# Kernel tuning notes

Hardware: AMD Instinct MI355X
Metric: run time of the kernel (lower is better)

The kernel has to match this reference:

```python
import jax, jax.numpy as jnp
import numpy as np

S = 3072      # total packed tokens
D = 1536      # hidden_size
H = 12        # num_heads
HD = D // H   # head_dim = 128
NSEQ = 4      # number of packed sequences (images)


def rotate_half(x):
    x1 = x[..., : x.shape[-1] // 2]
    x2 = x[..., x.shape[-1] // 2 :]
    return jnp.concatenate((-x2, x1), axis=-1)


def setup_inputs() -> dict:
    key = jax.random.key(0)
    k1, k2, k3 = jax.random.split(key, 3)
    hidden_states = jax.random.normal(k1, (S, D), jnp.float32)
    # 4 equal-length packed sequences
    cu_seqlens = (jnp.arange(NSEQ + 1, dtype=jnp.int32) * (S // NSEQ))
    # RoPE cos/sin per token, period within each packed sequence
    pos = (jnp.arange(S) % (S // NSEQ)).astype(jnp.float32)
    inv_freq = 1.0 / (10000.0 ** (jnp.arange(0, HD // 2, dtype=jnp.float32) / (HD // 2)))
    freqs = pos[:, None] * inv_freq[None, :]          # [S, HD//2]
    emb = jnp.concatenate([freqs, freqs], axis=-1)    # [S, HD]
    cos, sin = jnp.cos(emb), jnp.sin(emb)
    qkv_w = jax.random.normal(k2, (3 * D, D), jnp.float32) * (D ** -0.5)
    qkv_b = jnp.zeros((3 * D,), jnp.float32)
    proj_w = jax.random.normal(k3, (D, D), jnp.float32) * (D ** -0.5)
    return {
        "hidden_states": hidden_states,
        "cos": cos,
        "sin": sin,
        "qkv_w": qkv_w,
        "qkv_b": qkv_b,
        "proj_w": proj_w,
        "cu_seqlens": cu_seqlens,
    }


def reference(hidden_states, cos, sin, qkv_w, qkv_b, proj_w, cu_seqlens):
    s_len, dim = hidden_states.shape
    # fused QKV projection -> [S, 3, H, HD]
    qkv = (hidden_states @ qkv_w.T + qkv_b).reshape(s_len, 3, H, HD)
    q, k, v = qkv[:, 0], qkv[:, 1], qkv[:, 2]         # each [S, H, HD]
    # inline RoPE (fp32, broadcast over heads)
    c = cos[:, None, :].astype(jnp.float32)
    s = sin[:, None, :].astype(jnp.float32)
    qf, kf = q.astype(jnp.float32), k.astype(jnp.float32)
    q = (qf * c + rotate_half(qf) * s).astype(q.dtype)
    k = (kf * c + rotate_half(kf) * s).astype(k.dtype)
    # block-diagonal (varlen) mask from cu_seqlens
    seg = jnp.searchsorted(cu_seqlens, jnp.arange(s_len), side="right")  # [S]
    same_seq = seg[:, None] == seg[None, :]                              # [S, S]
    bias = jnp.where(same_seq, 0.0, -jnp.inf).astype(jnp.float32)
    scaling = HD ** -0.5
    # scores [H, S, S]
    scores = jnp.einsum("shd,thd->hst", q, k) * scaling + bias[None]
    probs = jax.nn.softmax(scores.astype(jnp.float32), axis=-1).astype(q.dtype)
    attn = jnp.einsum("hst,thd->shd", probs, v).reshape(s_len, dim)
    return attn @ proj_w.T
```

## Files before the change

kernel.cpp:

```cpp
#include <hip/hip_runtime.h>
#include <stdint.h>

#define S_LEN 3072
#define DIM   1536
#define NH    12
#define HD    128
#define QKV_N 4608

typedef unsigned short u16;
typedef __bf16 bf16x8 __attribute__((ext_vector_type(8)));
typedef float  f32x4  __attribute__((ext_vector_type(4)));
typedef u16    u16x8  __attribute__((ext_vector_type(8)));

#define AS1 __attribute__((address_space(1)))
#define AS3 __attribute__((address_space(3)))
#define GLL16(g, l) __builtin_amdgcn_global_load_lds((AS1 void*)(g), (AS3 void*)(l), 16, 0, 0)

__device__ __forceinline__ u16 f2bf(float f) {
  unsigned u = __float_as_uint(f);
  u = (u + 0x7fffu + ((u >> 16) & 1u)) >> 16;
  return (u16)u;
}
__device__ __forceinline__ float bf2f(u16 b) {
  return __uint_as_float(((unsigned)b) << 16);
}

__global__ __launch_bounds__(256) void cvt_bf16_3(const float* __restrict__ in0, u16* __restrict__ out0, int n0,
                                                  const float* __restrict__ in1, u16* __restrict__ out1, int n1,
                                                  const float* __restrict__ in2, u16* __restrict__ out2, int n2) {
  int total = n0 + n1 + n2;
  int stride = gridDim.x * blockDim.x;
  for (int i = blockIdx.x * blockDim.x + threadIdx.x; i < total; i += stride) {
    const float* src; u16* dst; int j;
    if (i < n0)           { src = in0; dst = out0; j = i; }
    else if (i < n0 + n1) { src = in1; dst = out1; j = i - n0; }
    else                  { src = in2; dst = out2; j = i - n0 - n1; }
    float4 v = ((const float4*)src)[j];
    ushort4 o;
    o.x = f2bf(v.x); o.y = f2bf(v.y); o.z = f2bf(v.z); o.w = f2bf(v.w);
    ((ushort4*)dst)[j] = o;
  }
}

__device__ __forceinline__ bf16x8 frag2(const u16* region, int row, int ch) {
  int L = row >> 1;
  int slot = ((ch + ((row & 1) << 2)) ^ L) & 7;
  return *(const bf16x8*)(region + L * 64 + slot * 8);
}

__global__ __launch_bounds__(512, 2) void gemm_bt_256(const u16* __restrict__ A,
                                                      const u16* __restrict__ B,
                                                      const float* __restrict__ bias,
                                                      u16* __restrict__ Cout,
                                                      int M, int N, int K) {
  __shared__ __attribute__((aligned(16))) u16 lds[8 * 8192];

  const int t = threadIdx.x;
  const int l = t & 63;
  const int w = t >> 6;
  const int wm = w >> 2;
  const int wn = w & 3;
  const int lr = l & 15;
  const int lc = l >> 4;

  const int nbx = N >> 8;
  const int nwg = gridDim.x;
  const int q = nwg >> 3, r = nwg & 7;
  const int xcd = blockIdx.x & 7, rest = blockIdx.x >> 3;
  const int wgid = (xcd < r ? xcd * (q + 1) : r * (q + 1) + (xcd - r) * q) + rest;
  const int m0 = (wgid / nbx) * 256;
  const int n0 = (wgid % nbx) * 256;

  const int nk = K >> 6;

  f32x4 acc[8][4];
  #pragma unroll
  for (int i = 0; i < 8; ++i)
    #pragma unroll
    for (int j = 0; j < 4; ++j) acc[i][j] = f32x4{0.f, 0.f, 0.f, 0.f};

  auto stage_half = [&](int buf, int ks, int ab, int kt) {
    const u16* base = ab ? B : A;
    const int x0 = ab ? n0 : m0;
    u16* dst = lds + (((buf << 2) | (ks << 1) | ab) * 8192);
    #pragma unroll
    for (int i = 0; i < 2; ++i) {
      int C = t + i * 512;
      int L = C >> 3, s = C & 7;
      int u = s ^ (L & 7);
      int row = 2 * L + (u >> 2), ch = u & 3;
      const u16* src = base + (size_t)(x0 + row) * K + kt * 64 + ks * 32 + ch * 8;
      GLL16(src, dst + C * 8);
    }
  };

  stage_half(0, 0, 0, 0); stage_half(0, 0, 1, 0);
  stage_half(0, 1, 0, 0); stage_half(0, 1, 1, 0);
  if (nk > 1) { stage_half(1, 0, 0, 1); stage_half(1, 0, 1, 1); }
  asm volatile("s_waitcnt vmcnt(4)" ::: "memory");
  __builtin_amdgcn_s_barrier();

  for (int kt = 0; kt < nk; ++kt) {
    const int buf = kt & 1, nbuf = buf ^ 1;
    const bool st1 = (kt + 1 < nk);
    const bool st2 = (kt + 2 < nk);

    const u16* A0 = lds + (((buf << 2) | 0) * 8192);
    const u16* B0 = lds + (((buf << 2) | 1) * 8192);
    const u16* A1 = lds + (((buf << 2) | 2) * 8192);
    const u16* B1 = lds + (((buf << 2) | 3) * 8192);

    bf16x8 bfrag[4], afr[4];

    #pragma unroll
    for (int ni = 0; ni < 4; ++ni) bfrag[ni] = frag2(B0, wn * 64 + ni * 16 + lr, lc);
    #pragma unroll
    for (int mi = 0; mi < 4; ++mi) afr[mi] = frag2(A0, wm * 128 + mi * 16 + lr, lc);
    if (st1) stage_half(nbuf, 1, 0, kt + 1);
    __builtin_amdgcn_s_barrier();
    __builtin_amdgcn_s_setprio(1);
    #pragma unroll
    for (int mi = 0; mi < 4; ++mi)
      #pragma unroll
      for (int ni = 0; ni < 4; ++ni)
        acc[mi][ni] = __builtin_amdgcn_mfma_f32_16x16x32_bf16(afr[mi], bfrag[ni],
                                                              acc[mi][ni], 0, 0, 0);
    __builtin_amdgcn_s_setprio(0);
    __builtin_amdgcn_s_barrier();

    #pragma unroll
    for (int mi = 0; mi < 4; ++mi) afr[mi] = frag2(A0, wm * 128 + 64 + mi * 16 + lr, lc);
    if (st1) stage_half(nbuf, 1, 1, kt + 1);
    __builtin_amdgcn_s_barrier();
    __builtin_amdgcn_s_setprio(1);
    #pragma unroll
    for (int mi = 0; mi < 4; ++mi)
      #pragma unroll
      for (int ni = 0; ni < 4; ++ni)
        acc[4 + mi][ni] = __builtin_amdgcn_mfma_f32_16x16x32_bf16(afr[mi], bfrag[ni],
                                                                  acc[4 + mi][ni], 0, 0, 0);
    __builtin_amdgcn_s_setprio(0);
    __builtin_amdgcn_s_barrier();

    #pragma unroll
    for (int ni = 0; ni < 4; ++ni) bfrag[ni] = frag2(B1, wn * 64 + ni * 16 + lr, lc);
    #pragma unroll
    for (int mi = 0; mi < 4; ++mi) afr[mi] = frag2(A1, wm * 128 + mi * 16 + lr, lc);
    if (st2) stage_half(buf, 0, 0, kt + 2);
    __builtin_amdgcn_s_barrier();
    __builtin_amdgcn_s_setprio(1);
    #pragma unroll
    for (int mi = 0; mi < 4; ++mi)
      #pragma unroll
      for (int ni = 0; ni < 4; ++ni)
        acc[mi][ni] = __builtin_amdgcn_mfma_f32_16x16x32_bf16(afr[mi], bfrag[ni],
                                                              acc[mi][ni], 0, 0, 0);
    __builtin_amdgcn_s_setprio(0);
    __builtin_amdgcn_s_barrier();

    #pragma unroll
    for (int mi = 0; mi < 4; ++mi) afr[mi] = frag2(A1, wm * 128 + 64 + mi * 16 + lr, lc);
    if (st2) {
      stage_half(buf, 0, 1, kt + 2);
      asm volatile("s_waitcnt vmcnt(4)" ::: "memory");
    } else if (st1) {
      asm volatile("s_waitcnt vmcnt(0)" ::: "memory");
    }
    __builtin_amdgcn_s_barrier();
    __builtin_amdgcn_s_setprio(1);
    #pragma unroll
    for (int mi = 0; mi < 4; ++mi)
      #pragma unroll
      for (int ni = 0; ni < 4; ++ni)
        acc[4 + mi][ni] = __builtin_amdgcn_mfma_f32_16x16x32_bf16(afr[mi], bfrag[ni],
                                                                  acc[4 + mi][ni], 0, 0, 0);
    __builtin_amdgcn_s_setprio(0);
    __builtin_amdgcn_s_barrier();
  }

  {
    float bv[4];
    #pragma unroll
    for (int ni = 0; ni < 4; ++ni)
      bv[ni] = bias ? bias[n0 + wn * 64 + ni * 16 + lr] : 0.f;
    #pragma unroll
    for (int mi = 0; mi < 8; ++mi) {
      int row = wm * 128 + mi * 16 + lc * 4;
      #pragma unroll
      for (int ni = 0; ni < 4; ++ni) {
        int scol = (wn * 64 + ni * 16 + lr) ^ (lc << 4);
        #pragma unroll
        for (int rr = 0; rr < 4; ++rr)
          lds[(row + rr) * 256 + scol] = f2bf(acc[mi][ni][rr] + bv[ni]);
      }
    }
    __syncthreads();
    #pragma unroll
    for (int i = 0; i < 16; ++i) {
      int id = i * 512 + t;
      int row = id >> 5, c16 = id & 31;
      int s = (row >> 2) & 3;
      u16x8 v = *(const u16x8*)(lds + row * 256 + ((c16 * 8) ^ (s << 4)));
      *(u16x8*)(Cout + (size_t)(m0 + row) * N + n0 + c16 * 8) = v;
    }
  }
}

__device__ __forceinline__ bf16x8 lds_frag(const u16* base, int row, int ch) {
  return *(const bf16x8*)(base + row * 64 + ((ch ^ row) & 7) * 8);
}

template <bool BIAS, bool OUTF32>
__global__ __launch_bounds__(256) void gemm_bt(const u16* __restrict__ A,
                                               const u16* __restrict__ B,
                                               const float* __restrict__ bias,
                                               void* __restrict__ Cout,
                                               int M, int N, int K) {
  __shared__ u16 Asm[128 * 64];
  __shared__ u16 Bsm[128 * 64];
  const int t = threadIdx.x;
  const int l = t & 63;
  const int w = t >> 6;
  const int wm = w >> 1, wn = w & 1;
  const int m0 = blockIdx.y * 128, n0 = blockIdx.x * 128;

  f32x4 acc[4][4];
  #pragma unroll
  for (int i = 0; i < 4; ++i)
    #pragma unroll
    for (int j = 0; j < 4; ++j) acc[i][j] = f32x4{0.f, 0.f, 0.f, 0.f};

  for (int k0 = 0; k0 < K; k0 += 64) {
    __syncthreads();
    #pragma unroll
    for (int r4 = 0; r4 < 4; ++r4) {
      int C = t + r4 * 256;
      int row = C >> 3, ch = C & 7;
      int sch = (ch ^ row) & 7;
      GLL16(A + (size_t)(m0 + row) * K + k0 + sch * 8, Asm + (size_t)C * 8);
      GLL16(B + (size_t)(n0 + row) * K + k0 + sch * 8, Bsm + (size_t)C * 8);
    }
    __syncthreads();
    #pragma unroll
    for (int ks = 0; ks < 2; ++ks) {
      bf16x8 af[4], bfr[4];
      #pragma unroll
      for (int mi = 0; mi < 4; ++mi)
        af[mi] = lds_frag(Asm, wm * 64 + mi * 16 + (l & 15), ks * 4 + (l >> 4));
      #pragma unroll
      for (int ni = 0; ni < 4; ++ni)
        bfr[ni] = lds_frag(Bsm, wn * 64 + ni * 16 + (l & 15), ks * 4 + (l >> 4));
      #pragma unroll
      for (int mi = 0; mi < 4; ++mi)
        #pragma unroll
        for (int ni = 0; ni < 4; ++ni)
          acc[mi][ni] = __builtin_amdgcn_mfma_f32_16x16x32_bf16(af[mi], bfr[ni],
                                                                acc[mi][ni], 0, 0, 0);
    }
  }

  #pragma unroll
  for (int ni = 0; ni < 4; ++ni) {
    int col = n0 + wn * 64 + ni * 16 + (l & 15);
    float bv = 0.f;
    if (BIAS) bv = bias[col];
    #pragma unroll
    for (int mi = 0; mi < 4; ++mi) {
      int rbase = m0 + wm * 64 + mi * 16 + ((l >> 4) << 2);
      #pragma unroll
      for (int rr = 0; rr < 4; ++rr) {
        float v = acc[mi][ni][rr] + bv;
        if (OUTF32)
          ((float*)Cout)[(size_t)(rbase + rr) * N + col] = v;
        else
          ((u16*)Cout)[(size_t)(rbase + rr) * N + col] = f2bf(v);
      }
    }
  }
}

__global__ __launch_bounds__(256) void rope_pack(const u16* __restrict__ QKV,
                                                 const float* __restrict__ cosb,
                                                 const float* __restrict__ sinb,
                                                 u16* __restrict__ Qp,
                                                 u16* __restrict__ Kp,
                                                 u16* __restrict__ Vt) {
  __shared__ u16 vtile[64][128];
  const int t = threadIdx.x;
  const int s0 = blockIdx.x * 64;
  const int h = blockIdx.y;

  const int srow = s0 + (t >> 2);
  const int d0 = (t & 3) * 16;
  const u16* qkvrow = QKV + (size_t)srow * QKV_N + h * HD;
  const float qscale = 0.08838834764831845f * 1.4426950408889634f;

  float cl[16], chh[16], sl[16], shh[16];
  #pragma unroll
  for (int g = 0; g < 4; ++g) {
    *(float4*)(cl + 4 * g)  = *(const float4*)(cosb + srow * HD + d0 + 4 * g);
    *(float4*)(chh + 4 * g) = *(const float4*)(cosb + srow * HD + d0 + 64 + 4 * g);
    *(float4*)(sl + 4 * g)  = *(const float4*)(sinb + srow * HD + d0 + 4 * g);
    *(float4*)(shh + 4 * g) = *(const float4*)(sinb + srow * HD + d0 + 64 + 4 * g);
  }

  #pragma unroll
  for (int which = 0; which < 2; ++which) {
    const u16* src = qkvrow + which * DIM;
    u16* dst = (which ? Kp : Qp) + ((size_t)h * S_LEN + srow) * HD;
    const float sc = which ? 1.f : qscale;
    u16x8 xl0 = *(const u16x8*)(src + d0);
    u16x8 xl1 = *(const u16x8*)(src + d0 + 8);
    u16x8 xh0 = *(const u16x8*)(src + d0 + 64);
    u16x8 xh1 = *(const u16x8*)(src + d0 + 72);
    u16x8 o0, o1, o2, o3;
    #pragma unroll
    for (int j = 0; j < 8; ++j) {
      float xlo = bf2f(xl0[j]), xhi = bf2f(xh0[j]);
      o0[j] = f2bf((xlo * cl[j] - xhi * sl[j]) * sc);
      o2[j] = f2bf((xhi * chh[j] + xlo * shh[j]) * sc);
      float xlo2 = bf2f(xl1[j]), xhi2 = bf2f(xh1[j]);
      o1[j] = f2bf((xlo2 * cl[j + 8] - xhi2 * sl[j + 8]) * sc);
      o3[j] = f2bf((xhi2 * chh[j + 8] + xlo2 * shh[j + 8]) * sc);
    }
    *(u16x8*)(dst + d0)      = o0;
    *(u16x8*)(dst + d0 + 8)  = o1;
    *(u16x8*)(dst + d0 + 64) = o2;
    *(u16x8*)(dst + d0 + 72) = o3;
  }

  #pragma unroll
  for (int r4 = 0; r4 < 4; ++r4) {
    int C = t + r4 * 256;
    int row = C >> 4, ch = C & 15;
    *(uint4*)(&vtile[row][ch * 8]) =
        *(const uint4*)(QKV + (size_t)(s0 + row) * QKV_N + 2 * DIM + h * HD + ch * 8);
  }
  __syncthreads();
  const int d = t >> 1;
  const int sc0 = (t & 1) * 32;
  u16* vdst = Vt + ((size_t)h * HD + d) * S_LEN + s0 + sc0;
  #pragma unroll
  for (int j = 0; j < 32; j += 8) {
    u16x8 v;
    #pragma unroll
    for (int e = 0; e < 8; ++e) v[e] = vtile[sc0 + j + e][d];
    *(u16x8*)(vdst + j) = v;
  }
}

__global__ __launch_bounds__(256) void attn_fwd(const u16* __restrict__ Qp,
                                                const u16* __restrict__ Kp,
                                                const u16* __restrict__ Vt,
                                                const int* __restrict__ cu,
                                                u16* __restrict__ Obf) {
  __shared__ u16 K_lds[2][64 * 128];
  __shared__ u16 VT_lds[2][128 * 64];
  __shared__ u16 P_lds[4][16 * 72];

  const int t = threadIdx.x;
  const int l = t & 63;
  const int w = t >> 6;
  const int q0 = blockIdx.x * 64;
  const int h = blockIdx.y;

  int cs = 0, ce = S_LEN;
  #pragma unroll
  for (int b = 0; b < 4; ++b) {
    int lo = cu[b], hi = cu[b + 1];
    if (q0 >= lo && q0 < hi) { cs = lo; ce = hi; }
  }

  const int qrow = q0 + w * 16 + (l & 15);
  bf16x8 qf[4];
  const u16* qptr = Qp + ((size_t)h * S_LEN + qrow) * HD + ((l >> 4) * 8);
  #pragma unroll
  for (int ks = 0; ks < 4; ++ks) qf[ks] = *(const bf16x8*)(qptr + ks * 32);

  f32x4 acc_o[8];
  #pragma unroll
  for (int i = 0; i < 8; ++i) acc_o[i] = f32x4{0.f, 0.f, 0.f, 0.f};
  float m_run[4], l_run[4];
  #pragma unroll
  for (int r = 0; r < 4; ++r) { m_run[r] = -1e30f; l_run[r] = 0.f; }

  auto stage = [&](int c, int kv0) {
    const u16* kbase = Kp + ((size_t)h * S_LEN + kv0) * HD;
    #pragma unroll
    for (int r4 = 0; r4 < 4; ++r4) {
      int C = t + r4 * 256;
      int row = C >> 4, ch = C & 15;
      int sch = (ch & 8) | ((ch ^ row) & 7);
      GLL16(kbase + row * HD + sch * 8, &K_lds[c][0] + (size_t)C * 8);
    }
    const u16* vbase = Vt + (size_t)h * HD * S_LEN + kv0;
    #pragma unroll
    for (int r4 = 0; r4 < 4; ++r4) {
      int C = t + r4 * 256;
      int row = C >> 3, ch = C & 7;
      int sch = (ch ^ row) & 7;
      GLL16(vbase + (size_t)row * S_LEN + sch * 8, &VT_lds[c][0] + (size_t)C * 8);
    }
  };

  const int nt = (ce - cs) >> 6;
  stage(0, cs);

  for (int it = 0; it < nt; ++it) {
    const int cur = it & 1;
    __builtin_amdgcn_s_barrier();
    if (it + 1 < nt) {
      stage(cur ^ 1, cs + (it + 1) * 64);
      asm volatile("s_waitcnt vmcnt(8)" ::: "memory");
    } else {
      asm volatile("s_waitcnt vmcnt(0)" ::: "memory");
    }
    __builtin_amdgcn_s_barrier();

    const u16* kb = &K_lds[cur][0];
    const u16* vb = &VT_lds[cur][0];

    f32x4 s_acc[4];
    __builtin_amdgcn_s_setprio(1);
    #pragma unroll
    for (int nf = 0; nf < 4; ++nf) {
      s_acc[nf] = f32x4{0.f, 0.f, 0.f, 0.f};
      int kcol = nf * 16 + (l & 15);
      #pragma unroll
      for (int ks = 0; ks < 4; ++ks) {
        int ch = ks * 4 + (l >> 4);
        int sch = (ch & 8) | ((ch ^ kcol) & 7);
        bf16x8 kf = *(const bf16x8*)(kb + kcol * 128 + sch * 8);
        s_acc[nf] = __builtin_amdgcn_mfma_f32_16x16x32_bf16(qf[ks], kf, s_acc[nf], 0, 0, 0);
      }
    }
    __builtin_amdgcn_s_setprio(0);

    float p[4][4], alpha[4];
    #pragma unroll
    for (int r = 0; r < 4; ++r) {
      float v = fmaxf(fmaxf(s_acc[0][r], s_acc[1][r]), fmaxf(s_acc[2][r], s_acc[3][r]));
      #pragma unroll
      for (int m = 1; m < 16; m <<= 1) v = fmaxf(v, __shfl_xor(v, m, 64));
      float mn = fmaxf(m_run[r], v);
      alpha[r] = __builtin_amdgcn_exp2f(m_run[r] - mn);
      m_run[r] = mn;
      float sum = 0.f;
      #pragma unroll
      for (int nf = 0; nf < 4; ++nf) {
        float pv = __builtin_amdgcn_exp2f(s_acc[nf][r] - mn);
        p[nf][r] = pv;
        sum += pv;
      }
      #pragma unroll
      for (int m = 1; m < 16; m <<= 1) sum += __shfl_xor(sum, m, 64);
      l_run[r] = l_run[r] * alpha[r] + sum;
    }
    #pragma unroll
    for (int onf = 0; onf < 8; ++onf)
      #pragma unroll
      for (int r = 0; r < 4; ++r) acc_o[onf][r] *= alpha[r];

    u16* pl = P_lds[w];
    #pragma unroll
    for (int nf = 0; nf < 4; ++nf)
      #pragma unroll
      for (int r = 0; r < 4; ++r)
        pl[((l >> 4) * 4 + r) * 72 + nf * 16 + (l & 15)] = f2bf(p[nf][r]);

    __builtin_amdgcn_s_setprio(1);
    #pragma unroll
    for (int ks = 0; ks < 2; ++ks) {
      bf16x8 pa = *(const bf16x8*)(pl + (l & 15) * 72 + ks * 32 + (l >> 4) * 8);
      #pragma unroll
      for (int onf = 0; onf < 8; ++onf) {
        int d = onf * 16 + (l & 15);
        int ch = ks * 4 + (l >> 4);
        int sch = (ch ^ d) & 7;
        bf16x8 vf = *(const bf16x8*)(vb + d * 64 + sch * 8);
        acc_o[onf] = __builtin_amdgcn_mfma_f32_16x16x32_bf16(pa, vf, acc_o[onf], 0, 0, 0);
      }
    }
    __builtin_amdgcn_s_setprio(0);
  }

  #pragma unroll
  for (int r = 0; r < 4; ++r) {
    float inv = 1.f / l_run[r];
    int srow = q0 + w * 16 + ((l >> 4) << 2) + r;
    u16* orow = Obf + (size_t)srow * DIM + h * HD + (l & 15);
    #pragma unroll
    for (int onf = 0; onf < 8; ++onf) orow[onf * 16] = f2bf(acc_o[onf][r] * inv);
  }
}

extern "C" void kernel_launch(void* const* d_in, const int* in_sizes, int n_in,
                              void* d_out, int out_size, void* d_ws, size_t ws_size,
                              hipStream_t stream) {
  const float* hidden = (const float*)d_in[0];
  const float* cosb   = (const float*)d_in[1];
  const float* sinb   = (const float*)d_in[2];
  const float* qkv_w  = (const float*)d_in[3];
  const float* qkv_b  = (const float*)d_in[4];
  const float* proj_w = (const float*)d_in[5];
  const int*   cu     = (const int*)d_in[6];

  u16* Hbf   = (u16*)d_ws;
  u16* Wqkv  = Hbf   + (size_t)S_LEN * DIM;
  u16* Wproj = Wqkv  + (size_t)QKV_N * DIM;
  u16* QKVbf = Wproj + (size_t)DIM * DIM;
  u16* Kp    = QKVbf + (size_t)S_LEN * QKV_N;
  u16* Vt    = Kp    + (size_t)NH * S_LEN * HD;
  u16* Qp    = Wqkv;
  u16* Abf   = Hbf;

  cvt_bf16_3<<<2048, 256, 0, stream>>>(hidden, Hbf, S_LEN * DIM / 4,
                                       qkv_w, Wqkv, QKV_N * DIM / 4,
                                       proj_w, Wproj, DIM * DIM / 4);

  gemm_bt_256<<<(S_LEN / 256) * (QKV_N / 256), 512, 0, stream>>>(
      Hbf, Wqkv, qkv_b, QKVbf, S_LEN, QKV_N, DIM);

  rope_pack<<<dim3(S_LEN / 64, NH), 256, 0, stream>>>(QKVbf, cosb, sinb, Qp, Kp, Vt);

  attn_fwd<<<dim3(S_LEN / 64, NH), 256, 0, stream>>>(Qp, Kp, Vt, cu, Abf);

  gemm_bt<false, true><<<dim3(DIM / 128, S_LEN / 128), 256, 0, stream>>>(
      Abf, Wproj, nullptr, d_out, S_LEN, DIM, DIM);
}
```

Baseline: 174.1 us.

## Read V fragments directly from global memory instead of staging through LDS

Removes the double-buffered LDS staging of the transposed V tile and loads V MFMA operands straight from global memory in the PV loop. This aims to cut LDS capacity and traffic and the staging instructions, and it adjusts the async wait count to match. The cost is that global-load latency now sits in the inner MFMA loop without prefetch, and the four waves no longer share V data through LDS. The P scratch row stride is also changed to alter bank mapping.

```diff
diff --git a/kernel.cpp b/kernel.cpp
--- a/kernel.cpp
+++ b/kernel.cpp
@@ -355,12 +355,13 @@
                                                 const int* __restrict__ cu,
                                                 u16* __restrict__ Obf) {
   __shared__ u16 K_lds[2][64 * 128];
-  __shared__ u16 VT_lds[2][128 * 64];
-  __shared__ u16 P_lds[4][16 * 72];
+  __shared__ u16 P_lds[4][16 * 76];
 
   const int t = threadIdx.x;
   const int l = t & 63;
   const int w = t >> 6;
+  const int lr = l & 15;
+  const int lq = l >> 4;
   const int q0 = blockIdx.x * 64;
   const int h = blockIdx.y;
 
@@ -371,11 +372,13 @@
     if (q0 >= lo && q0 < hi) { cs = lo; ce = hi; }
   }
 
-  const int qrow = q0 + w * 16 + (l & 15);
+  const int qrow = q0 + w * 16 + lr;
   bf16x8 qf[4];
-  const u16* qptr = Qp + ((size_t)h * S_LEN + qrow) * HD + ((l >> 4) * 8);
+  const u16* qptr = Qp + ((size_t)h * S_LEN + qrow) * HD + lq * 8;
   #pragma unroll
   for (int ks = 0; ks < 4; ++ks) qf[ks] = *(const bf16x8*)(qptr + ks * 32);
+
+  const u16* vhead = Vt + (size_t)h * HD * S_LEN;
 
   f32x4 acc_o[8];
   #pragma unroll
@@ -393,14 +396,6 @@
       int sch = (ch & 8) | ((ch ^ row) & 7);
       GLL16(kbase + row * HD + sch * 8, &K_lds[c][0] + (size_t)C * 8);
     }
-    const u16* vbase = Vt + (size_t)h * HD * S_LEN + kv0;
-    #pragma unroll
-    for (int r4 = 0; r4 < 4; ++r4) {
-      int C = t + r4 * 256;
-      int row = C >> 3, ch = C & 7;
-      int sch = (ch ^ row) & 7;
-      GLL16(vbase + (size_t)row * S_LEN + sch * 8, &VT_lds[c][0] + (size_t)C * 8);
-    }
   };
 
   const int nt = (ce - cs) >> 6;
@@ -408,27 +403,27 @@
 
   for (int it = 0; it < nt; ++it) {
     const int cur = it & 1;
+    const int kv0 = cs + it * 64;
     __builtin_amdgcn_s_barrier();
     if (it + 1 < nt) {
-      stage(cur ^ 1, cs + (it + 1) * 64);
-      asm volatile("s_waitcnt vmcnt(8)" ::: "memory");
+      stage(cur ^ 1, kv0 + 64);
+      asm volatile("s_waitcnt vmcnt(4)" ::: "memory");
     } else {
       asm volatile("s_waitcnt vmcnt(0)" ::: "memory");
     }
     __builtin_amdgcn_s_barrier();
 
     const u16* kb = &K_lds[cur][0];
-    const u16* vb = &VT_lds[cur][0];
 
     f32x4 s_acc[4];
     __builtin_amdgcn_s_setprio(1);
     #pragma unroll
     for (int nf = 0; nf < 4; ++nf) {
       s_acc[nf] = f32x4{0.f, 0.f, 0.f, 0.f};
-      int kcol = nf * 16 + (l & 15);
+      int kcol = nf * 16 + lr;
       #pragma unroll
       for (int ks = 0; ks < 4; ++ks) {
-        int ch = ks * 4 + (l >> 4);
+        int ch = ks * 4 + lq;
         int sch = (ch & 8) | ((ch ^ kcol) & 7);
         bf16x8 kf = *(const bf16x8*)(kb + kcol * 128 + sch * 8);
         s_acc[nf] = __builtin_amdgcn_mfma_f32_16x16x32_bf16(qf[ks], kf, s_acc[nf], 0, 0, 0);
@@ -466,18 +461,17 @@
     for (int nf = 0; nf < 4; ++nf)
       #pragma unroll
       for (int r = 0; r < 4; ++r)
-        pl[((l >> 4) * 4 + r) * 72 + nf * 16 + (l & 15)] = f2bf(p[nf][r]);
+        pl[(lq * 4 + r) * 76 + nf * 16 + lr] = f2bf(p[nf][r]);
 
     __builtin_amdgcn_s_setprio(1);
     #pragma unroll
     for (int ks = 0; ks < 2; ++ks) {
-      bf16x8 pa = *(const bf16x8*)(pl + (l & 15) * 72 + ks * 32 + (l >> 4) * 8);
+      bf16x8 pa = *(const bf16x8*)(pl + lr * 76 + ks * 32 + lq * 8);
       #pragma unroll
       for (int onf = 0; onf < 8; ++onf) {
-        int d = onf * 16 + (l & 15);
-        int ch = ks * 4 + (l >> 4);
-        int sch = (ch ^ d) & 7;
-        bf16x8 vf = *(const bf16x8*)(vb + d * 64 + sch * 8);
+        int d = onf * 16 + lr;
+        int ch = ks * 4 + lq;
+        bf16x8 vf = *(const bf16x8*)(vhead + (size_t)d * S_LEN + kv0 + ch * 8);
         acc_o[onf] = __builtin_amdgcn_mfma_f32_16x16x32_bf16(pa, vf, acc_o[onf], 0, 0, 0);
       }
     }
@@ -487,8 +481,8 @@
   #pragma unroll
   for (int r = 0; r < 4; ++r) {
     float inv = 1.f / l_run[r];
-    int srow = q0 + w * 16 + ((l >> 4) << 2) + r;
-    u16* orow = Obf + (size_t)srow * DIM + h * HD + (l & 15);
+    int srow = q0 + w * 16 + (lq << 2) + r;
+    u16* orow = Obf + (size_t)srow * DIM + h * HD + lr;
     #pragma unroll
     for (int onf = 0; onf < 8; ++onf) orow[onf * 16] = f2bf(acc_o[onf][r] * inv);
   }
```

After: 206.4 us. 18.6% more time.
